# Kernel optimization log

Measured on AMD Instinct MI355X. Metric: run time of the kernel, lower is better.

The kernel has to match this reference:

```python
import jax, jax.numpy as jnp
import numpy as np

MARGIN = 0.5        # contrastive margin (init kwarg)
NUM_LABELS = 20     # label ids are in [0, NUM_LABELS)


def setup_inputs() -> dict:
    key = jax.random.key(0)
    k1, k2 = jax.random.split(key)
    emb = jax.random.normal(k1, (4, 16, 64, 64), dtype=jnp.float32)
    lab = jax.random.randint(k2, (4, 64, 64), 0, NUM_LABELS, dtype=jnp.int32)
    return {"emb": emb, "lab": lab}


def _loss_one(x, y):
    # x: (C, H, W) embedding, y: (H, W) int labels
    C, H, W = x.shape
    N = H * W
    xf = x.reshape(C, N)
    # per-pixel centering across channels, then L2-normalize across channels
    xc = xf - jnp.mean(xf, axis=0, keepdims=True)
    nrm = jnp.sqrt(jnp.sum(xc * xc, axis=0))           # (N,)
    denom = jnp.where(nrm > 0, nrm, 1.0)
    e = jnp.where(nrm > 0, xc / denom, 0.0).T          # (N, C); NaN-mask -> 0
    sim = (e @ e.T) * 0.5 + 0.5                        # (N, N) in [0, 1]

    yi = y.reshape(N)
    yf = yi.astype(jnp.float32) + 1.0
    eq = yf[:, None] == yf[None, :]
    nz = (yf[:, None] * yf[None, :]) != 0.0            # product-zero exclusion (faithful)
    lp = jnp.where(nz, jnp.where(eq, 1.0, -1.0), 0.0)  # label-pair matrix

    # inverse-frequency per-pixel weights, outer product for pairs
    cnt = jnp.zeros((NUM_LABELS,), jnp.float32).at[yi].add(1.0)
    wpix = 1.0 / cnt[yi]                               # (N,)
    Wm = wpix[:, None] * wpix[None, :]                 # (N, N)

    # positive pairs: relu(1 - sim); negative pairs: relu(sim - margin)
    loss = jnp.where(lp == 1.0, jnp.maximum(1.0 - sim, 0.0),
                     jnp.where(lp == -1.0, jnp.maximum(sim - MARGIN, 0.0), 0.0))
    return jnp.sum(Wm * loss) / N


def reference(emb, lab):
    return jnp.sum(jax.vmap(_loss_one)(emb, lab))
```

## Files before the change

### kernel.cpp

```cpp
#include <hip/hip_runtime.h>

#define NUM_LABELS 20
#define N_PIX 4096
#define C_DIM 16
#define BATCH 4

#define PTILE 128
#define PNT (N_PIX / PTILE)
#define PTPAIRS (PNT * (PNT + 1) / 2)
#define NPAIRBLK (BATCH * PTPAIRS)

#define PREP_SLICES 16
#define KPAD 24

typedef __attribute__((ext_vector_type(8))) short bf16x8;
typedef __attribute__((ext_vector_type(4))) float f32x4;

__device__ __forceinline__ unsigned int bf16rne(float f) {
    unsigned int x = __float_as_uint(f);
    return (x + 0x7fffu + ((x >> 16) & 1u)) >> 16;
}

__global__ __launch_bounds__(256) void prep_kernel(
    const float* __restrict__ emb,
    const int*   __restrict__ lab,
    unsigned short* __restrict__ gT,
    float* __restrict__ w_out)
{
    const int blk = blockIdx.x;
    const int b  = blk / PREP_SLICES;
    const int sl = blk % PREP_SLICES;
    const int t  = threadIdx.x;
    const int wv = t >> 6;

    __shared__ int   hist[4][NUM_LABELS];
    __shared__ float rinv[NUM_LABELS];
    __shared__ float xt[C_DIM][256];

    for (int i = t; i < 4 * NUM_LABELS; i += 256) (&hist[0][0])[i] = 0;
    __syncthreads();

    const int* yb = lab + (size_t)b * N_PIX;
    for (int n = t; n < N_PIX; n += 256) atomicAdd(&hist[wv][yb[n]], 1);

    const float* xb = emb + (size_t)b * C_DIM * N_PIX + sl * 256;
#pragma unroll
    for (int c = 0; c < C_DIM; ++c) xt[c][t] = xb[(size_t)c * N_PIX + t];
    __syncthreads();

    if (t < NUM_LABELS) {
        const int c = hist[0][t] + hist[1][t] + hist[2][t] + hist[3][t];
        rinv[t] = (c > 0) ? 1.0f / (float)c : 0.0f;
    }
    __syncthreads();

    const int n = sl * 256 + t;
    float v[C_DIM];
    float s = 0.f;
#pragma unroll
    for (int c = 0; c < C_DIM; ++c) { v[c] = xt[c][t]; s += v[c]; }
    const float mean = s * (1.0f / C_DIM);
    float ss = 0.f;
#pragma unroll
    for (int c = 0; c < C_DIM; ++c) { v[c] -= mean; ss += v[c] * v[c]; }
    const float nrm = sqrtf(ss);
    const float wv2 = rinv[yb[n]];
    const float inv = (nrm > 0.f) ? (wv2 / nrm) : 0.f;

    unsigned int u[8];
#pragma unroll
    for (int k = 0; k < 8; ++k) {
        const unsigned int lo = bf16rne(v[2 * k] * inv);
        const unsigned int hi = bf16rne(v[2 * k + 1] * inv);
        u[k] = lo | (hi << 16);
    }
    unsigned int* gp = (unsigned int*)(gT + ((size_t)b * N_PIX + n) * C_DIM);
    *reinterpret_cast<uint4*>(gp)     = make_uint4(u[0], u[1], u[2], u[3]);
    *reinterpret_cast<uint4*>(gp + 4) = make_uint4(u[4], u[5], u[6], u[7]);
    w_out[(size_t)b * N_PIX + n] = wv2;
}

__global__ __launch_bounds__(256) void pair_kernel(
    const unsigned short* __restrict__ gT,
    const float* __restrict__ w,
    const int*   __restrict__ lab,
    float* __restrict__ partials)
{
    const int k0 = blockIdx.x % PTPAIRS;
    const int b  = blockIdx.x / PTPAIRS;

    const float nn = (float)PNT;
    int ti = (int)(((2.f * nn + 1.f) -
                    sqrtf((2.f * nn + 1.f) * (2.f * nn + 1.f) - 8.f * (float)k0)) * 0.5f);
    if (ti < 0) ti = 0;
    if (ti > PNT - 1) ti = PNT - 1;
    auto rowoff = [](int r) { return r * PNT - (r * (r - 1)) / 2; };
    while (ti > 0 && k0 < rowoff(ti)) --ti;
    while (ti < PNT - 1 && k0 >= rowoff(ti + 1)) ++ti;
    const int tj = ti + (k0 - rowoff(ti));
    const bool diag = (ti == tj);

    __shared__ unsigned short sI[PTILE * KPAD];
    __shared__ unsigned short sJ[PTILE * KPAD];
    __shared__ float swI[PTILE], swJ[PTILE];
    __shared__ int   syI[PTILE], syJ[PTILE];

    const int t = threadIdx.x;
    const unsigned short* gb = gT + (size_t)b * N_PIX * C_DIM;

    {
        const int row = t >> 1, half = t & 1;
        const uint4 vI = *(reinterpret_cast<const uint4*>(gb + (size_t)(ti * PTILE + row) * C_DIM) + half);
        const uint4 vJ = *(reinterpret_cast<const uint4*>(gb + (size_t)(tj * PTILE + row) * C_DIM) + half);
        *reinterpret_cast<uint4*>(&sI[row * KPAD + half * 8]) = vI;
        *reinterpret_cast<uint4*>(&sJ[row * KPAD + half * 8]) = vJ;
    }
    if (t < PTILE) {
        swI[t] = w[(size_t)b * N_PIX + ti * PTILE + t];
        syI[t] = lab[(size_t)b * N_PIX + ti * PTILE + t];
    } else {
        const int u = t - PTILE;
        swJ[u] = w[(size_t)b * N_PIX + tj * PTILE + u];
        syJ[u] = lab[(size_t)b * N_PIX + tj * PTILE + u];
    }
    __syncthreads();

    const int wv   = t >> 6;
    const int lane = t & 63;
    const int lo16 = lane & 15;
    const int hi   = lane >> 4;
    const bool doread = (hi < 2);

    bf16x8 afrag[2] = {bf16x8{}, bf16x8{}};
    int    yIr[2][4];
    float  wIr[2][4];
#pragma unroll
    for (int rt = 0; rt < 2; ++rt) {
        const int rtile = wv * 2 + rt;
        if (doread)
            afrag[rt] = *reinterpret_cast<const bf16x8*>(&sI[(rtile * 16 + lo16) * KPAD + hi * 8]);
        const int rbase = rtile * 16 + hi * 4;
#pragma unroll
        for (int j = 0; j < 4; ++j) { yIr[rt][j] = syI[rbase + j]; wIr[rt][j] = swI[rbase + j]; }
    }

    float sum = 0.f;
#pragma unroll
    for (int ct = 0; ct < 8; ++ct) {
        bf16x8 bfrag = bf16x8{};
        if (doread)
            bfrag = *reinterpret_cast<const bf16x8*>(&sJ[(ct * 16 + lo16) * KPAD + hi * 8]);
        const int   yq = syJ[ct * 16 + lo16];
        const float wq = swJ[ct * 16 + lo16];
#pragma unroll
        for (int rt = 0; rt < 2; ++rt) {
            const int rtile = wv * 2 + rt;
            if (diag && rtile > ct) continue;
            f32x4 acc = {0.f, 0.f, 0.f, 0.f};
            acc = __builtin_amdgcn_mfma_f32_16x16x32_bf16(afrag[rt], bfrag, acc, 0, 0, 0);
            if (diag && rtile == ct) {
#pragma unroll
                for (int j = 0; j < 4; ++j) {
                    const float s  = acc[j];
                    const float v  = (yIr[rt][j] == yq) ? fmaf(wIr[rt][j], wq, -s) : fmaxf(s, 0.f);
                    const int iloc = hi * 4 + j;
                    const float f  = (iloc < lo16) ? 1.f : ((iloc == lo16) ? 0.5f : 0.f);
                    sum += f * v;
                }
            } else {
#pragma unroll
                for (int j = 0; j < 4; ++j) {
                    const float s = acc[j];
                    sum += (yIr[rt][j] == yq) ? fmaf(wIr[rt][j], wq, -s) : fmaxf(s, 0.f);
                }
            }
        }
    }

#pragma unroll
    for (int off = 32; off > 0; off >>= 1) sum += __shfl_down(sum, off);
    __shared__ float wred[4];
    if (lane == 0) wred[wv] = sum;
    __syncthreads();
    if (t == 0) partials[blockIdx.x] = wred[0] + wred[1] + wred[2] + wred[3];
}

__global__ __launch_bounds__(256) void reduce_kernel(
    const float* __restrict__ partials, int n, float* __restrict__ out)
{
    __shared__ double sd[256];
    const int t = threadIdx.x;
    double s = 0.0;
    for (int i = t; i < n; i += 256) s += (double)partials[i];
    sd[t] = s;
    __syncthreads();
#pragma unroll
    for (int k = 128; k > 0; k >>= 1) {
        if (t < k) sd[t] += sd[t + k];
        __syncthreads();
    }
    if (t == 0) out[0] = (float)(sd[0] * (1.0 / (double)N_PIX));
}

extern "C" void kernel_launch(void* const* d_in, const int* in_sizes, int n_in,
                              void* d_out, int out_size, void* d_ws, size_t ws_size,
                              hipStream_t stream) {
    const float* emb = (const float*)d_in[0];
    const int*   lab = (const int*)d_in[1];
    float* out = (float*)d_out;

    unsigned short* gT = (unsigned short*)d_ws;
    float* w_buf    = (float*)(gT + (size_t)BATCH * N_PIX * C_DIM);
    float* partials = w_buf + (size_t)BATCH * N_PIX;

    prep_kernel<<<BATCH * PREP_SLICES, 256, 0, stream>>>(emb, lab, gT, w_buf);
    pair_kernel<<<NPAIRBLK, 256, 0, stream>>>(gT, w_buf, lab, partials);
    reduce_kernel<<<1, 256, 0, stream>>>(partials, NPAIRBLK, out);
}
```

Measured before the change: 22.62 us.

## Fold same-label weight term into closed form and drop per-pixel weights from pair kernel

Same-label pairs contribute w_i*w_j - s. Summed over label classes, the w_i*w_j part is a constant: 0.5 per present label over the upper triangle. The diagonal self-term is handled through a per-slice sum of squared scaled norms computed in the prep kernel. This removes the weight buffer, its shared-memory staging and its per-element loads and FMAs from the pair kernel, and it also simplifies the diagonal mask and vectorises the label loads. The cost is extra reductions in prep and reduce, plus some rounding difference from using bf16 products on the diagonal.

```diff
diff --git a/kernel.cpp b/kernel.cpp
--- a/kernel.cpp
+++ b/kernel.cpp
@@ -11,6 +11,7 @@
 #define NPAIRBLK (BATCH * PTPAIRS)
 
 #define PREP_SLICES 16
+#define NPREP (BATCH * PREP_SLICES)
 #define KPAD 24
 
 typedef __attribute__((ext_vector_type(8))) short bf16x8;
@@ -25,17 +26,20 @@
     const float* __restrict__ emb,
     const int*   __restrict__ lab,
     unsigned short* __restrict__ gT,
-    float* __restrict__ w_out)
+    float* __restrict__ sliceSq,
+    float* __restrict__ presF)
 {
     const int blk = blockIdx.x;
     const int b  = blk / PREP_SLICES;
     const int sl = blk % PREP_SLICES;
     const int t  = threadIdx.x;
     const int wv = t >> 6;
+    const int lane = t & 63;
 
     __shared__ int   hist[4][NUM_LABELS];
     __shared__ float rinv[NUM_LABELS];
     __shared__ float xt[C_DIM][256];
+    __shared__ float wsum[4];
 
     for (int i = t; i < 4 * NUM_LABELS; i += 256) (&hist[0][0])[i] = 0;
     __syncthreads();
@@ -54,6 +58,14 @@
     }
     __syncthreads();
 
+    if (sl == 0 && t == 0) {
+        int p = 0;
+#pragma unroll
+        for (int l = 0; l < NUM_LABELS; ++l)
+            p += (rinv[l] > 0.f) ? 1 : 0;
+        presF[b] = (float)p;
+    }
+
     const int n = sl * 256 + t;
     float v[C_DIM];
     float s = 0.f;
@@ -64,8 +76,8 @@
 #pragma unroll
     for (int c = 0; c < C_DIM; ++c) { v[c] -= mean; ss += v[c] * v[c]; }
     const float nrm = sqrtf(ss);
-    const float wv2 = rinv[yb[n]];
-    const float inv = (nrm > 0.f) ? (wv2 / nrm) : 0.f;
+    const float w   = rinv[yb[n]];
+    const float inv = (nrm > 0.f) ? (w / nrm) : 0.f;
 
     unsigned int u[8];
 #pragma unroll
@@ -77,12 +89,17 @@
     unsigned int* gp = (unsigned int*)(gT + ((size_t)b * N_PIX + n) * C_DIM);
     *reinterpret_cast<uint4*>(gp)     = make_uint4(u[0], u[1], u[2], u[3]);
     *reinterpret_cast<uint4*>(gp + 4) = make_uint4(u[4], u[5], u[6], u[7]);
-    w_out[(size_t)b * N_PIX + n] = wv2;
+
+    float sq = inv * inv * ss;
+#pragma unroll
+    for (int off = 32; off > 0; off >>= 1) sq += __shfl_down(sq, off);
+    if (lane == 0) wsum[wv] = sq;
+    __syncthreads();
+    if (t == 0) sliceSq[blk] = wsum[0] + wsum[1] + wsum[2] + wsum[3];
 }
 
 __global__ __launch_bounds__(256) void pair_kernel(
     const unsigned short* __restrict__ gT,
-    const float* __restrict__ w,
     const int*   __restrict__ lab,
     float* __restrict__ partials)
 {
@@ -102,8 +119,7 @@
 
     __shared__ unsigned short sI[PTILE * KPAD];
     __shared__ unsigned short sJ[PTILE * KPAD];
-    __shared__ float swI[PTILE], swJ[PTILE];
-    __shared__ int   syI[PTILE], syJ[PTILE];
+    __shared__ int syI[PTILE], syJ[PTILE];
 
     const int t = threadIdx.x;
     const unsigned short* gb = gT + (size_t)b * N_PIX * C_DIM;
@@ -116,11 +132,9 @@
         *reinterpret_cast<uint4*>(&sJ[row * KPAD + half * 8]) = vJ;
     }
     if (t < PTILE) {
-        swI[t] = w[(size_t)b * N_PIX + ti * PTILE + t];
         syI[t] = lab[(size_t)b * N_PIX + ti * PTILE + t];
     } else {
         const int u = t - PTILE;
-        swJ[u] = w[(size_t)b * N_PIX + tj * PTILE + u];
         syJ[u] = lab[(size_t)b * N_PIX + tj * PTILE + u];
     }
     __syncthreads();
@@ -133,15 +147,13 @@
 
     bf16x8 afrag[2] = {bf16x8{}, bf16x8{}};
     int    yIr[2][4];
-    float  wIr[2][4];
 #pragma unroll
     for (int rt = 0; rt < 2; ++rt) {
         const int rtile = wv * 2 + rt;
         if (doread)
             afrag[rt] = *reinterpret_cast<const bf16x8*>(&sI[(rtile * 16 + lo16) * KPAD + hi * 8]);
-        const int rbase = rtile * 16 + hi * 4;
-#pragma unroll
-        for (int j = 0; j < 4; ++j) { yIr[rt][j] = syI[rbase + j]; wIr[rt][j] = swI[rbase + j]; }
+        const int4 yv = *reinterpret_cast<const int4*>(&syI[rtile * 16 + hi * 4]);
+        yIr[rt][0] = yv.x; yIr[rt][1] = yv.y; yIr[rt][2] = yv.z; yIr[rt][3] = yv.w;
     }
 
     float sum = 0.f;
@@ -150,8 +162,7 @@
         bf16x8 bfrag = bf16x8{};
         if (doread)
             bfrag = *reinterpret_cast<const bf16x8*>(&sJ[(ct * 16 + lo16) * KPAD + hi * 8]);
-        const int   yq = syJ[ct * 16 + lo16];
-        const float wq = swJ[ct * 16 + lo16];
+        const int yq = syJ[ct * 16 + lo16];
 #pragma unroll
         for (int rt = 0; rt < 2; ++rt) {
             const int rtile = wv * 2 + rt;
@@ -161,17 +172,18 @@
             if (diag && rtile == ct) {
 #pragma unroll
                 for (int j = 0; j < 4; ++j) {
-                    const float s  = acc[j];
-                    const float v  = (yIr[rt][j] == yq) ? fmaf(wIr[rt][j], wq, -s) : fmaxf(s, 0.f);
+                    const float s = acc[j];
+                    const float r = fmaxf(s, 0.f);
+                    const float v = (yIr[rt][j] == yq) ? -s : r;
                     const int iloc = hi * 4 + j;
-                    const float f  = (iloc < lo16) ? 1.f : ((iloc == lo16) ? 0.5f : 0.f);
-                    sum += f * v;
+                    sum += (iloc < lo16) ? v : 0.f;
                 }
             } else {
 #pragma unroll
                 for (int j = 0; j < 4; ++j) {
                     const float s = acc[j];
-                    sum += (yIr[rt][j] == yq) ? fmaf(wIr[rt][j], wq, -s) : fmaxf(s, 0.f);
+                    const float r = fmaxf(s, 0.f);
+                    sum += (yIr[rt][j] == yq) ? -s : r;
                 }
             }
         }
@@ -186,12 +198,17 @@
 }
 
 __global__ __launch_bounds__(256) void reduce_kernel(
-    const float* __restrict__ partials, int n, float* __restrict__ out)
+    const float* __restrict__ partials,
+    const float* __restrict__ sliceSq,
+    const float* __restrict__ presF,
+    float* __restrict__ out)
 {
     __shared__ double sd[256];
     const int t = threadIdx.x;
     double s = 0.0;
-    for (int i = t; i < n; i += 256) s += (double)partials[i];
+    for (int i = t; i < NPAIRBLK; i += 256) s += (double)partials[i];
+    if (t < NPREP) s -= 0.5 * (double)sliceSq[t];
+    if (t < BATCH) s += 0.5 * (double)presF[t];
     sd[t] = s;
     __syncthreads();
 #pragma unroll
@@ -210,10 +227,11 @@
     float* out = (float*)d_out;
 
     unsigned short* gT = (unsigned short*)d_ws;
-    float* w_buf    = (float*)(gT + (size_t)BATCH * N_PIX * C_DIM);
-    float* partials = w_buf + (size_t)BATCH * N_PIX;
-
-    prep_kernel<<<BATCH * PREP_SLICES, 256, 0, stream>>>(emb, lab, gT, w_buf);
-    pair_kernel<<<NPAIRBLK, 256, 0, stream>>>(gT, w_buf, lab, partials);
-    reduce_kernel<<<1, 256, 0, stream>>>(partials, NPAIRBLK, out);
-}
+    float* sliceSq  = (float*)(gT + (size_t)BATCH * N_PIX * C_DIM);
+    float* presF    = sliceSq + NPREP;
+    float* partials = presF + BATCH;
+
+    prep_kernel<<<NPREP, 256, 0, stream>>>(emb, lab, gT, sliceSq, presF);
+    pair_kernel<<<NPAIRBLK, 256, 0, stream>>>(gT, lab, partials);
+    reduce_kernel<<<1, 256, 0, stream>>>(partials, sliceSq, presF, out);
+}
```

Result: no change. 22.58 us (-0.2%).
